# Optimization experiments

Measured on AMD Instinct MI355X. Metric: run time of the kernel, lower is better.

## Reference

```python
import jax, jax.numpy as jnp
import numpy as np

B, T, D = 2, 2048, 1024
H, HD = 16, 64  # num_heads, num_hiddens_per_head


def setup_inputs() -> dict:
    key = jax.random.key(0)
    ks = jax.random.split(key, 6)
    scale = 1.0 / np.sqrt(D)
    inputs_q = jax.random.normal(ks[0], (B, T, D), dtype=jnp.float32)
    inputs_kv = jax.random.normal(ks[1], (B, T, D), dtype=jnp.float32)
    # causal mask, broadcastable to [b, h, t, T]
    mask = jnp.tril(jnp.ones((T, T), dtype=bool))[None, None, :, :]
    Wq = jax.random.normal(ks[2], (D, H * HD), dtype=jnp.float32) * scale
    Wk = jax.random.normal(ks[3], (D, H * HD), dtype=jnp.float32) * scale
    Wv = jax.random.normal(ks[4], (D, H * HD), dtype=jnp.float32) * scale
    Wo = jax.random.normal(ks[5], (H * HD, D), dtype=jnp.float32) * scale
    return {"inputs_q": inputs_q, "inputs_kv": inputs_kv, "mask": mask,
            "Wq": Wq, "Wk": Wk, "Wv": Wv, "Wo": Wo}


def reference(inputs_q, inputs_kv, mask, Wq, Wk, Wv, Wo):
    b, t, _ = inputs_q.shape
    q = (inputs_q @ Wq).reshape(b, -1, H, HD)
    k = (inputs_kv @ Wk).reshape(b, -1, H, HD)
    v = (inputs_kv @ Wv).reshape(b, -1, H, HD)
    scores = jnp.einsum('bthd,bThd->bhtT', q, k) * (1.0 / jnp.sqrt(HD))
    scores = jnp.where(mask, scores, jnp.finfo(jnp.float32).min)
    attn = jax.nn.softmax(scores, axis=-1)
    out = jnp.einsum('bhtT,bThd->bthd', attn, v).reshape(b, t, H * HD)
    return out @ Wo
```

## Files before the change

### kernel.cpp

```cpp
#include <hip/hip_runtime.h>
#include <hip/hip_bf16.h>

#define B_  2
#define T_  2048
#define D_  1024
#define H_  16
#define HD_ 64

typedef __bf16 bf16x8 __attribute__((ext_vector_type(8)));
typedef float  f32x4  __attribute__((ext_vector_type(4)));

#define MFIX2  11.5415603f
#define QSCALE 0.18033688f

__device__ __forceinline__ __bf16 f2b(float f) {
  __hip_bfloat16 h = __float2bfloat16(f);
  return *reinterpret_cast<__bf16*>(&h);
}

__device__ __forceinline__ void gload_lds16(const __bf16* g, __bf16* l) {
  __builtin_amdgcn_global_load_lds((const unsigned int*)g, (unsigned int*)l, 16, 0, 0);
}

__global__ __launch_bounds__(256) void prep_k(const float* __restrict__ Xq,
                                              const float* __restrict__ Xkv,
                                              const float* __restrict__ Wq,
                                              const float* __restrict__ Wk,
                                              const float* __restrict__ Wv,
                                              const float* __restrict__ Wo,
                                              __hip_bfloat16* __restrict__ Xq_b,
                                              __hip_bfloat16* __restrict__ Xkv_b,
                                              __hip_bfloat16* __restrict__ WTall,
                                              __hip_bfloat16* __restrict__ WoT) {
  const int blk = blockIdx.x;
  if (blk < 8192) {
    const float* x = (blk < 4096) ? Xq : Xkv;
    __hip_bfloat16* y = (blk < 4096) ? Xq_b : Xkv_b;
    const size_t i = ((size_t)(blk & 4095) * 256 + threadIdx.x) * 4;
    f32x4 v = *(const f32x4*)(x + i);
    union { ushort4 u; __hip_bfloat16 h[4]; } o;
#pragma unroll
    for (int j = 0; j < 4; ++j) o.h[j] = __float2bfloat16(v[j]);
    *(ushort4*)(y + i) = o.u;
    return;
  }
  __shared__ float tile[64][65];
  const int wid  = (blk - 8192) >> 8;
  const int tid_ = (blk - 8192) & 255;
  const float* in = (wid == 0) ? Wq : (wid == 1) ? Wk : (wid == 2) ? Wv : Wo;
  __hip_bfloat16* out = (wid == 3) ? WoT : (WTall + (size_t)wid * 1024 * D_);
  const int bx = (tid_ & 15) * 64, by = (tid_ >> 4) * 64;
  const int tx = threadIdx.x & 63, ty = threadIdx.x >> 6;
#pragma unroll
  for (int i = ty; i < 64; i += 4)
    tile[i][tx] = in[(size_t)(by + i) * D_ + bx + tx];
  __syncthreads();
#pragma unroll
  for (int i = ty; i < 64; i += 4)
    out[(size_t)(bx + i) * D_ + by + tx] = __float2bfloat16(tile[tx][i]);
}

__global__ __launch_bounds__(256) void gemm_qkv_k(const __bf16* __restrict__ Aq,
                                                  const __bf16* __restrict__ Akv,
                                                  const __bf16* __restrict__ WTall,
                                                  __hip_bfloat16* __restrict__ Qd,
                                                  __hip_bfloat16* __restrict__ Kd,
                                                  __hip_bfloat16* __restrict__ Vd) {
  __shared__ __align__(16) __bf16 Al[128 * 32];
  __shared__ __align__(16) __bf16 Bl[128 * 32];
  __shared__ __align__(16) __bf16 Tr[64][136];

  const int bm = blockIdx.x * 128;
  const int bn = blockIdx.y * 128;
  const int w  = bn >> 10;
  const __bf16* A = (w == 0) ? Aq : Akv;

  const int wave = threadIdx.x >> 6, lane = threadIdx.x & 63;
  const int wm = (wave >> 1) * 64, wn = (wave & 1) * 64;
  const int lo = lane & 15, qh = lane >> 4;

  const int srow = threadIdx.x >> 2;
  const int skc  = (threadIdx.x & 3) * 8;
  const __bf16* Ag0 = A      + (size_t)(bm + srow) * D_ + skc;
  const __bf16* Bg0 = WTall  + (size_t)(bn + srow) * D_ + skc;
  __bf16* Al0 = Al + threadIdx.x * 8;
  __bf16* Bl0 = Bl + threadIdx.x * 8;

  f32x4 acc[4][4] = {};

  for (int k0 = 0; k0 < D_; k0 += 32) {
    __syncthreads();
    gload_lds16(Ag0 + k0,           Al0);
    gload_lds16(Ag0 + 64 * D_ + k0, Al0 + 64 * 32);
    gload_lds16(Bg0 + k0,           Bl0);
    gload_lds16(Bg0 + 64 * D_ + k0, Bl0 + 64 * 32);
    __syncthreads();

    bf16x8 af[4], bfr[4];
#pragma unroll
    for (int mt = 0; mt < 4; ++mt)
      af[mt] = *(const bf16x8*)(Al + (wm + mt * 16 + lo) * 32 + qh * 8);
#pragma unroll
    for (int nt = 0; nt < 4; ++nt)
      bfr[nt] = *(const bf16x8*)(Bl + (wn + nt * 16 + lo) * 32 + qh * 8);
#pragma unroll
    for (int mt = 0; mt < 4; ++mt)
#pragma unroll
      for (int nt = 0; nt < 4; ++nt)
        acc[mt][nt] = __builtin_amdgcn_mfma_f32_16x16x32_bf16(af[mt], bfr[nt], acc[mt][nt], 0, 0, 0);
  }

  if (w == 2) {
    const int bV  = bm >> 11;
    const int tV0 = bm & (T_ - 1);
#pragma unroll
    for (int ph = 0; ph < 2; ++ph) {
      __syncthreads();
      if ((wn >> 6) == ph) {
#pragma unroll
        for (int mt = 0; mt < 4; ++mt)
#pragma unroll
          for (int nt = 0; nt < 4; ++nt)
#pragma unroll
            for (int r = 0; r < 4; ++r)
              Tr[nt * 16 + lo][wm + mt * 16 + 4 * qh + r] = f2b(acc[mt][nt][r]);
      }
      __syncthreads();
      const int hcol = ((bn & 1023) >> 6) + ph;
      const int row  = threadIdx.x >> 2;
      const int tc   = (threadIdx.x & 3) * 32;
      __hip_bfloat16* dst = Vd + (((size_t)(bV * H_ + hcol) * HD_ + row) * T_) + tV0 + tc;
#pragma unroll
      for (int j = 0; j < 32; j += 8)
        *(bf16x8*)(__bf16*)(dst + j) = *(const bf16x8*)&Tr[row][tc + j];
    }
  } else {
    __hip_bfloat16* dst = (w == 0) ? Qd : Kd;
    const float scale = (w == 0) ? QSCALE : 1.0f;
    const int col0 = (bn + wn) & 1023;
#pragma unroll
    for (int mt = 0; mt < 4; ++mt)
#pragma unroll
      for (int nt = 0; nt < 4; ++nt)
#pragma unroll
        for (int r = 0; r < 4; ++r) {
          const int m = bm + wm + mt * 16 + 4 * qh + r;
          const int n = col0 + nt * 16 + lo;
          const int b = m >> 11, t = m & (T_ - 1);
          const int h = n >> 6,  d = n & 63;
          dst[(((size_t)(b * H_ + h) * T_ + t) << 6) + d] =
              __float2bfloat16(acc[mt][nt][r] * scale);
        }
  }
}

__global__ __launch_bounds__(256) void gemm_out_k(const __bf16* __restrict__ A,
                                                  const __bf16* __restrict__ Bt,
                                                  float* __restrict__ C) {
  __shared__ __align__(16) __bf16 Al[128 * 32];
  __shared__ __align__(16) __bf16 Bl[64 * 32];

  const int bm = blockIdx.x * 128;
  const int bn = blockIdx.y * 64;
  const int wave = threadIdx.x >> 6, lane = threadIdx.x & 63;
  const int wm = (wave >> 1) * 64, wn = (wave & 1) * 32;
  const int lo = lane & 15, qh = lane >> 4;

  const int srow = threadIdx.x >> 2;
  const int skc  = (threadIdx.x & 3) * 8;
  const __bf16* Ag0 = A  + (size_t)(bm + srow) * D_ + skc;
  const __bf16* Bg0 = Bt + (size_t)(bn + srow) * D_ + skc;
  __bf16* Al0 = Al + threadIdx.x * 8;
  __bf16* Bl0 = Bl + threadIdx.x * 8;

  f32x4 acc[4][2] = {};

  for (int k0 = 0; k0 < D_; k0 += 32) {
    __syncthreads();
    gload_lds16(Ag0 + k0,           Al0);
    gload_lds16(Ag0 + 64 * D_ + k0, Al0 + 64 * 32);
    gload_lds16(Bg0 + k0,           Bl0);
    __syncthreads();

    bf16x8 af[4], bfr[2];
#pragma unroll
    for (int mt = 0; mt < 4; ++mt)
      af[mt] = *(const bf16x8*)(Al + (wm + mt * 16 + lo) * 32 + qh * 8);
#pragma unroll
    for (int nt = 0; nt < 2; ++nt)
      bfr[nt] = *(const bf16x8*)(Bl + (wn + nt * 16 + lo) * 32 + qh * 8);
#pragma unroll
    for (int mt = 0; mt < 4; ++mt)
#pragma unroll
      for (int nt = 0; nt < 2; ++nt)
        acc[mt][nt] = __builtin_amdgcn_mfma_f32_16x16x32_bf16(af[mt], bfr[nt], acc[mt][nt], 0, 0, 0);
  }

#pragma unroll
  for (int mt = 0; mt < 4; ++mt)
#pragma unroll
    for (int nt = 0; nt < 2; ++nt)
#pragma unroll
      for (int r = 0; r < 4; ++r) {
        const int m = bm + wm + mt * 16 + 4 * qh + r;
        const int n = bn + wn + nt * 16 + lo;
        C[(size_t)m * D_ + n] = acc[mt][nt][r];
      }
}

__global__ __launch_bounds__(256, 2) void attn_slice_k(const __hip_bfloat16* __restrict__ Q,
                                                       const __hip_bfloat16* __restrict__ K,
                                                       const __hip_bfloat16* __restrict__ Vt,
                                                       __hip_bfloat16* __restrict__ Po,
                                                       float* __restrict__ Lp,
                                                       __hip_bfloat16* __restrict__ AO) {
  __shared__ __align__(16) __bf16 Kl[2][64 * 64];
  __shared__ __align__(16) __bf16 Vl[2][64 * 64];
  __shared__ __align__(16) __bf16 Pl[4][64][64];

  const int bh = blockIdx.x;
  const int u  = blockIdx.y;
  int qi, sl;
  if (u < 2)       { qi = u;                   sl = 0; }
  else if (u < 6)  { qi = 2 + ((u - 2) >> 1);  sl = (u - 2) & 1; }
  else if (u < 12) { qi = 4 + (u - 6) / 3;     sl = (u - 6) % 3; }
  else             { qi = 6 + ((u - 12) >> 2); sl = (u - 12) & 3; }
  const int n_i = 4 * qi + 4;
  const int jt0 = sl * 8;
  const int jt_end = (jt0 + 8 < n_i) ? jt0 + 8 : n_i;
  const int t0 = qi * 256;

  const int wave = threadIdx.x >> 6, lane = threadIdx.x & 63;
  const int lo = lane & 15, qh = lane >> 4;
  const int qw0 = t0 + wave * 64;
  const int wlast = 4 * qi + wave;

  const __hip_bfloat16* Qb = Q + (size_t)bh * T_ * HD_;
  const __bf16* Kb = (const __bf16*)(K  + (size_t)bh * T_ * HD_);
  const __bf16* Vb = (const __bf16*)(Vt + (size_t)bh * HD_ * T_);

  const int srow = threadIdx.x >> 3;
  const int ssc  = (threadIdx.x & 7) ^ (srow & 7);

#define STAGE(buf, jb2)                                                                     \
  do {                                                                                      \
    gload_lds16(Kb + (size_t)((jb2) + srow) * HD_ + ssc * 8,      Kl[(buf)] + threadIdx.x * 8);        \
    gload_lds16(Kb + (size_t)((jb2) + 32 + srow) * HD_ + ssc * 8, Kl[(buf)] + 2048 + threadIdx.x * 8); \
    gload_lds16(Vb + (size_t)srow * T_ + (jb2) + ssc * 8,         Vl[(buf)] + threadIdx.x * 8);        \
    gload_lds16(Vb + (size_t)(32 + srow) * T_ + (jb2) + ssc * 8,  Vl[(buf)] + 2048 + threadIdx.x * 8); \
  } while (0)

  bf16x8 qf[4][2];
#pragma unroll
  for (int mt = 0; mt < 4; ++mt)
#pragma unroll
    for (int ks = 0; ks < 2; ++ks)
      qf[mt][ks] = *(const bf16x8*)(Qb + (size_t)(qw0 + mt * 16 + lo) * HD_ + ks * 32 + qh * 8);

  const int rc0 = qh ^ (lo & 7);
  const int rc1 = (4 + qh) ^ (lo & 7);

  f32x4 o[4][4] = {};
  float lp[16] = {};

  STAGE(0, jt0 * 64);
  __syncthreads();
  int cur = 0;

  for (int jt = jt0; jt < jt_end; ++jt) {
    const int jb = jt * 64;
    if (jt + 1 < jt_end) STAGE(cur ^ 1, jb + 64);

    if (jt <= wlast) {
      bf16x8 kf[4][2];
#pragma unroll
      for (int nt = 0; nt < 4; ++nt) {
        kf[nt][0] = *(const bf16x8*)(Kl[cur] + (nt * 16 + lo) * 64 + rc0 * 8);
        kf[nt][1] = *(const bf16x8*)(Kl[cur] + (nt * 16 + lo) * 64 + rc1 * 8);
      }
#pragma unroll
      for (int mt = 0; mt < 4; ++mt) {
        const int qrb = qw0 + mt * 16;
        if (jb > qrb + 15) continue;
        f32x4 s[4];
#pragma unroll
        for (int nt = 0; nt < 4; ++nt) {
          const int j0 = jb + nt * 16;
          if (j0 > qrb + 15) { s[nt] = (f32x4){-1e30f, -1e30f, -1e30f, -1e30f}; continue; }
          f32x4 acc = {0.f, 0.f, 0.f, 0.f};
          acc = __builtin_amdgcn_mfma_f32_16x16x32_bf16(qf[mt][0], kf[nt][0], acc, 0, 0, 0);
          acc = __builtin_amdgcn_mfma_f32_16x16x32_bf16(qf[mt][1], kf[nt][1], acc, 0, 0, 0);
          if (j0 + 15 > qrb) {
#pragma unroll
            for (int r = 0; r < 4; ++r)
              if (j0 + lo > qrb + 4 * qh + r) acc[r] = -1e30f;
          }
          s[nt] = acc;
        }
#pragma unroll
        for (int nt = 0; nt < 4; ++nt)
#pragma unroll
          for (int r = 0; r < 4; ++r) {
            const float p = __builtin_amdgcn_exp2f(s[nt][r] - MFIX2);
            lp[mt * 4 + r] += p;
            Pl[wave][mt * 16 + 4 * qh + r]
              [(((2 * nt) + (lo >> 3)) ^ ((4 * qh + r) & 7)) * 8 + (lo & 7)] = f2b(p);
          }
      }
      bf16x8 vf[2][4];
#pragma unroll
      for (int nt = 0; nt < 4; ++nt) {
        vf[0][nt] = *(const bf16x8*)(Vl[cur] + (nt * 16 + lo) * 64 + rc0 * 8);
        vf[1][nt] = *(const bf16x8*)(Vl[cur] + (nt * 16 + lo) * 64 + rc1 * 8);
      }
#pragma unroll
      for (int mt = 0; mt < 4; ++mt) {
        if (jb > qw0 + mt * 16 + 15) continue;
        bf16x8 pf0 = *(const bf16x8*)&Pl[wave][mt * 16 + lo][rc0 * 8];
        bf16x8 pf1 = *(const bf16x8*)&Pl[wave][mt * 16 + lo][rc1 * 8];
#pragma unroll
        for (int nt = 0; nt < 4; ++nt) {
          o[mt][nt] = __builtin_amdgcn_mfma_f32_16x16x32_bf16(pf0, vf[0][nt], o[mt][nt], 0, 0, 0);
          o[mt][nt] = __builtin_amdgcn_mfma_f32_16x16x32_bf16(pf1, vf[1][nt], o[mt][nt], 0, 0, 0);
        }
      }
    }
    __syncthreads();
    cur ^= 1;
  }
#undef STAGE

#pragma unroll
  for (int i = 0; i < 16; ++i)
#pragma unroll
    for (int msk = 1; msk < 16; msk <<= 1)
      lp[i] += __shfl_xor(lp[i], msk, 64);

  if (u < 2) {
    const int b = bh >> 4, h = bh & 15;
#pragma unroll
    for (int mt = 0; mt < 4; ++mt)
#pragma unroll
      for (int nt = 0; nt < 4; ++nt)
#pragma unroll
        for (int r = 0; r < 4; ++r) {
          const int q = qw0 + mt * 16 + 4 * qh + r;
          AO[((size_t)(b * T_ + q) << 10) + h * 64 + nt * 16 + lo] =
              __float2bfloat16(o[mt][nt][r] / lp[mt * 4 + r]);
        }
  } else {
    __hip_bfloat16* base = Po + ((size_t)(bh * 20 + u) * 256 + wave * 64) * 64;
#pragma unroll
    for (int mt = 0; mt < 4; ++mt)
#pragma unroll
      for (int nt = 0; nt < 4; ++nt)
#pragma unroll
        for (int r = 0; r < 4; ++r)
          base[(mt * 16 + 4 * qh + r) * 64 + nt * 16 + lo] = __float2bfloat16(o[mt][nt][r]);
    if (lo == 0) {
      float* lpb = Lp + (size_t)(bh * 20 + u) * 256 + wave * 64;
#pragma unroll
      for (int mt = 0; mt < 4; ++mt)
#pragma unroll
        for (int r = 0; r < 4; ++r)
          lpb[mt * 16 + 4 * qh + r] = lp[mt * 4 + r];
    }
  }
}

__global__ __launch_bounds__(256) void attn_combine_k(const __hip_bfloat16* __restrict__ Po,
                                                      const float* __restrict__ Lp,
                                                      __hip_bfloat16* __restrict__ O) {
  const int bh = blockIdx.x;
  const int y  = blockIdx.y;
  const int qi = 2 + (y >> 3);
  const int rb = (y & 7) * 32;
  const int ns = (qi >> 1) + 1;
  const int ubase = (qi < 4) ? 2 + 2 * (qi - 2)
                  : (qi < 6) ? 6 + 3 * (qi - 4)
                  : 12 + 4 * (qi - 6);
  const int d8  = (threadIdx.x & 7) * 8;
  const int row = rb + (threadIdx.x >> 3);
  const int b = bh >> 4, h = bh & 15;
  const __bf16* ub = (const __bf16*)(Po + (size_t)(bh * 20 + ubase) * 16384);
  const float* lb = Lp + (size_t)(bh * 20 + ubase) * 256;

  float acc[8] = {};
  float l = 0.f;
  for (int s = 0; s < ns; ++s) {
    bf16x8 v = *(const bf16x8*)(ub + (size_t)s * 16384 + row * 64 + d8);
#pragma unroll
    for (int j = 0; j < 8; ++j) acc[j] += (float)v[j];
    l += lb[s * 256 + row];
  }
  const float rl = 1.0f / l;
  union { bf16x8 v; __bf16 h[8]; } ou;
#pragma unroll
  for (int j = 0; j < 8; ++j) ou.h[j] = f2b(acc[j] * rl);
  const int t = qi * 256 + row;
  *(bf16x8*)((__bf16*)O + (((size_t)(b * T_ + t)) << 10) + h * 64 + d8) = ou.v;
}

extern "C" void kernel_launch(void* const* d_in, const int* in_sizes, int n_in,
                              void* d_out, int out_size, void* d_ws, size_t ws_size,
                              hipStream_t stream) {
  const float* Xq  = (const float*)d_in[0];
  const float* Xkv = (const float*)d_in[1];
  const float* Wq  = (const float*)d_in[3];
  const float* Wk  = (const float*)d_in[4];
  const float* Wv  = (const float*)d_in[5];
  const float* Wo  = (const float*)d_in[6];

  char* ws = (char*)d_ws;
  const size_t MB = 1024ull * 1024ull;
  __hip_bfloat16* WTall = (__hip_bfloat16*)(ws + 0 * MB);
  __hip_bfloat16* WoT   = (__hip_bfloat16*)(ws + 6 * MB);
  __hip_bfloat16* Qw    = (__hip_bfloat16*)(ws + 8 * MB);
  __hip_bfloat16* Kw    = (__hip_bfloat16*)(ws + 16 * MB);
  __hip_bfloat16* Vw    = (__hip_bfloat16*)(ws + 24 * MB);
  __hip_bfloat16* AO    = (__hip_bfloat16*)(ws + 32 * MB);
  __hip_bfloat16* Po    = (__hip_bfloat16*)(ws + 40 * MB);
  float*          Lpart = (float*)        (ws + 62 * MB);
  __hip_bfloat16* Xq_b  = (__hip_bfloat16*)(ws + 84 * MB);
  __hip_bfloat16* Xkv_b = (__hip_bfloat16*)(ws + 92 * MB);

  const dim3 tb(256);

  prep_k<<<dim3(9216), tb, 0, stream>>>(Xq, Xkv, Wq, Wk, Wv, Wo,
                                        Xq_b, Xkv_b, WTall, WoT);

  gemm_qkv_k<<<dim3(32, 24), tb, 0, stream>>>((const __bf16*)Xq_b, (const __bf16*)Xkv_b,
                                              (const __bf16*)WTall, Qw, Kw, Vw);

  attn_slice_k<<<dim3(B_ * H_, 20), tb, 0, stream>>>(Qw, Kw, Vw, Po, Lpart, AO);
  attn_combine_k<<<dim3(B_ * H_, 48), tb, 0, stream>>>(Po, Lpart, AO);

  gemm_out_k<<<dim3(32, 16), tb, 0, stream>>>((const __bf16*)AO, (const __bf16*)WoT,
                                              (float*)d_out);
}
```

Baseline: 216.7 us.

## Load K/V fragments directly from global memory instead of LDS double-buffering

The attention kernel no longer stages K and V tiles into shared memory with async global-to-LDS loads. Each wave now reads its MFMA operand fragments straight from global memory (relying on L1/L2) and loops only up to its own causal limit. This drops the block-wide __syncthreads, frees LDS, and lets waves run independently. The cost is that the four waves fetch the same K/V data redundantly and lose the prefetch overlap.

New measurement: 225.7 us. 4.2% more time.

```diff
diff --git a/kernel.cpp b/kernel.cpp
--- a/kernel.cpp
+++ b/kernel.cpp
@@ -214,8 +214,6 @@
                                                        __hip_bfloat16* __restrict__ Po,
                                                        float* __restrict__ Lp,
                                                        __hip_bfloat16* __restrict__ AO) {
-  __shared__ __align__(16) __bf16 Kl[2][64 * 64];
-  __shared__ __align__(16) __bf16 Vl[2][64 * 64];
   __shared__ __align__(16) __bf16 Pl[4][64][64];
 
   const int bh = blockIdx.x;
@@ -234,22 +232,12 @@
   const int lo = lane & 15, qh = lane >> 4;
   const int qw0 = t0 + wave * 64;
   const int wlast = 4 * qi + wave;
+  const int my_end = (jt_end < wlast + 1) ? jt_end : wlast + 1;
 
   const __hip_bfloat16* Qb = Q + (size_t)bh * T_ * HD_;
   const __bf16* Kb = (const __bf16*)(K  + (size_t)bh * T_ * HD_);
   const __bf16* Vb = (const __bf16*)(Vt + (size_t)bh * HD_ * T_);
 
-  const int srow = threadIdx.x >> 3;
-  const int ssc  = (threadIdx.x & 7) ^ (srow & 7);
-
-#define STAGE(buf, jb2)                                                                     \
-  do {                                                                                      \
-    gload_lds16(Kb + (size_t)((jb2) + srow) * HD_ + ssc * 8,      Kl[(buf)] + threadIdx.x * 8);        \
-    gload_lds16(Kb + (size_t)((jb2) + 32 + srow) * HD_ + ssc * 8, Kl[(buf)] + 2048 + threadIdx.x * 8); \
-    gload_lds16(Vb + (size_t)srow * T_ + (jb2) + ssc * 8,         Vl[(buf)] + threadIdx.x * 8);        \
-    gload_lds16(Vb + (size_t)(32 + srow) * T_ + (jb2) + ssc * 8,  Vl[(buf)] + 2048 + threadIdx.x * 8); \
-  } while (0)
-
   bf16x8 qf[4][2];
 #pragma unroll
   for (int mt = 0; mt < 4; ++mt)
@@ -263,72 +251,66 @@
   f32x4 o[4][4] = {};
   float lp[16] = {};
 
-  STAGE(0, jt0 * 64);
-  __syncthreads();
-  int cur = 0;
-
-  for (int jt = jt0; jt < jt_end; ++jt) {
+  for (int jt = jt0; jt < my_end; ++jt) {
     const int jb = jt * 64;
-    if (jt + 1 < jt_end) STAGE(cur ^ 1, jb + 64);
-
-    if (jt <= wlast) {
-      bf16x8 kf[4][2];
+
+    bf16x8 kf[4][2];
+#pragma unroll
+    for (int nt = 0; nt < 4; ++nt) {
+      const __bf16* kr = Kb + (size_t)(jb + nt * 16 + lo) * HD_ + qh * 8;
+      kf[nt][0] = *(const bf16x8*)(kr);
+      kf[nt][1] = *(const bf16x8*)(kr + 32);
+    }
+
+#pragma unroll
+    for (int mt = 0; mt < 4; ++mt) {
+      const int qrb = qw0 + mt * 16;
+      if (jb > qrb + 15) continue;
+      f32x4 s[4];
 #pragma unroll
       for (int nt = 0; nt < 4; ++nt) {
-        kf[nt][0] = *(const bf16x8*)(Kl[cur] + (nt * 16 + lo) * 64 + rc0 * 8);
-        kf[nt][1] = *(const bf16x8*)(Kl[cur] + (nt * 16 + lo) * 64 + rc1 * 8);
+        const int j0 = jb + nt * 16;
+        if (j0 > qrb + 15) { s[nt] = (f32x4){-1e30f, -1e30f, -1e30f, -1e30f}; continue; }
+        f32x4 acc = {0.f, 0.f, 0.f, 0.f};
+        acc = __builtin_amdgcn_mfma_f32_16x16x32_bf16(qf[mt][0], kf[nt][0], acc, 0, 0, 0);
+        acc = __builtin_amdgcn_mfma_f32_16x16x32_bf16(qf[mt][1], kf[nt][1], acc, 0, 0, 0);
+        if (j0 + 15 > qrb) {
+#pragma unroll
+          for (int r = 0; r < 4; ++r)
+            if (j0 + lo > qrb + 4 * qh + r) acc[r] = -1e30f;
+        }
+        s[nt] = acc;
       }
 #pragma unroll
-      for (int mt = 0; mt < 4; ++mt) {
-        const int qrb = qw0 + mt * 16;
-        if (jb > qrb + 15) continue;
-        f32x4 s[4];
-#pragma unroll
-        for (int nt = 0; nt < 4; ++nt) {
-          const int j0 = jb + nt * 16;
-          if (j0 > qrb + 15) { s[nt] = (f32x4){-1e30f, -1e30f, -1e30f, -1e30f}; continue; }
-          f32x4 acc = {0.f, 0.f, 0.f, 0.f};
-          acc = __builtin_amdgcn_mfma_f32_16x16x32_bf16(qf[mt][0], kf[nt][0], acc, 0, 0, 0);
-          acc = __builtin_amdgcn_mfma_f32_16x16x32_bf16(qf[mt][1], kf[nt][1], acc, 0, 0, 0);
-          if (j0 + 15 > qrb) {
-#pragma unroll
-            for (int r = 0; r < 4; ++r)
-              if (j0 + lo > qrb + 4 * qh + r) acc[r] = -1e30f;
-          }
-          s[nt] = acc;
+      for (int nt = 0; nt < 4; ++nt)
+#pragma unroll
+        for (int r = 0; r < 4; ++r) {
+          const float p = __builtin_amdgcn_exp2f(s[nt][r] - MFIX2);
+          lp[mt * 4 + r] += p;
+          Pl[wave][mt * 16 + 4 * qh + r]
+            [(((2 * nt) + (lo >> 3)) ^ ((4 * qh + r) & 7)) * 8 + (lo & 7)] = f2b(p);
         }
-#pragma unroll
-        for (int nt = 0; nt < 4; ++nt)
-#pragma unroll
-          for (int r = 0; r < 4; ++r) {
-            const float p = __builtin_amdgcn_exp2f(s[nt][r] - MFIX2);
-            lp[mt * 4 + r] += p;
-            Pl[wave][mt * 16 + 4 * qh + r]
-              [(((2 * nt) + (lo >> 3)) ^ ((4 * qh + r) & 7)) * 8 + (lo & 7)] = f2b(p);
-          }
+    }
+
+    bf16x8 vf[2][4];
+#pragma unroll
+    for (int nt = 0; nt < 4; ++nt) {
+      const __bf16* vr = Vb + (size_t)(nt * 16 + lo) * T_ + jb + qh * 8;
+      vf[0][nt] = *(const bf16x8*)(vr);
+      vf[1][nt] = *(const bf16x8*)(vr + 32);
+    }
+#pragma unroll
+    for (int mt = 0; mt < 4; ++mt) {
+      if (jb > qw0 + mt * 16 + 15) continue;
+      bf16x8 pf0 = *(const bf16x8*)&Pl[wave][mt * 16 + lo][rc0 * 8];
+      bf16x8 pf1 = *(const bf16x8*)&Pl[wave][mt * 16 + lo][rc1 * 8];
+#pragma unroll
+      for (int nt = 0; nt < 4; ++nt) {
+        o[mt][nt] = __builtin_amdgcn_mfma_f32_16x16x32_bf16(pf0, vf[0][nt], o[mt][nt], 0, 0, 0);
+        o[mt][nt] = __builtin_amdgcn_mfma_f32_16x16x32_bf16(pf1, vf[1][nt], o[mt][nt], 0, 0, 0);
       }
-      bf16x8 vf[2][4];
-#pragma unroll
-      for (int nt = 0; nt < 4; ++nt) {
-        vf[0][nt] = *(const bf16x8*)(Vl[cur] + (nt * 16 + lo) * 64 + rc0 * 8);
-        vf[1][nt] = *(const bf16x8*)(Vl[cur] + (nt * 16 + lo) * 64 + rc1 * 8);
-      }
-#pragma unroll
-      for (int mt = 0; mt < 4; ++mt) {
-        if (jb > qw0 + mt * 16 + 15) continue;
-        bf16x8 pf0 = *(const bf16x8*)&Pl[wave][mt * 16 + lo][rc0 * 8];
-        bf16x8 pf1 = *(const bf16x8*)&Pl[wave][mt * 16 + lo][rc1 * 8];
-#pragma unroll
-        for (int nt = 0; nt < 4; ++nt) {
-          o[mt][nt] = __builtin_amdgcn_mfma_f32_16x16x32_bf16(pf0, vf[0][nt], o[mt][nt], 0, 0, 0);
-          o[mt][nt] = __builtin_amdgcn_mfma_f32_16x16x32_bf16(pf1, vf[1][nt], o[mt][nt], 0, 0, 0);
-        }
-      }
-    }
-    __syncthreads();
-    cur ^= 1;
-  }
-#undef STAGE
+    }
+  }
 
 #pragma unroll
   for (int i = 0; i < 16; ++i)
```
